# Performance work log

Measured on AMD Instinct MI355X. Metric: run time of the kernel, lower is better.

The kernel has to match this reference:

```python
import jax, jax.numpy as jnp
import numpy as np

T_IN, T_OUT = 16, 25          # in_length, out_length
B, K = 4096, 32               # heroes, neighbors per hero
N = B * K                     # total neighbor tracks
ENC, DEC, DYN, EMB = 64, 128, 32, 32


def _lrelu(x):
    return jnp.where(x >= 0, x, 0.1 * x)


def _lstm(x, Wih, Whh, bih, bhh, hidden):
    """PyTorch-convention LSTM (gate order i,f,g,o). x: [T, B, D]. Returns (all_h [T,B,H], last_h [B,H])."""
    z = jnp.zeros((x.shape[1], hidden), x.dtype)

    def step(carry, xt):
        h, c = carry
        g = xt @ Wih.T + bih + h @ Whh.T + bhh
        i, f, gg, o = jnp.split(g, 4, axis=-1)
        c = jax.nn.sigmoid(f) * c + jax.nn.sigmoid(i) * jnp.tanh(gg)
        h = jax.nn.sigmoid(o) * jnp.tanh(c)
        return (h, c), h

    (h, c), hs = jax.lax.scan(step, (z, z), x)
    return hs, h


def setup_inputs() -> dict:
    key = jax.random.key(0)
    ks = jax.random.split(key, 20)
    p = lambda k, s: jax.random.normal(k, s, jnp.float32) * 0.1
    return {
        "hist": jax.random.normal(ks[0], (T_IN, B, 2), jnp.float32),
        "nbrs": jax.random.normal(ks[1], (T_IN, N, 2), jnp.float32),
        "Wip": p(ks[2], (EMB, 2)), "bip": p(ks[3], (EMB,)),
        "Wih_e": p(ks[4], (4 * ENC, EMB)), "Whh_e": p(ks[5], (4 * ENC, ENC)),
        "bih_e": p(ks[6], (4 * ENC,)), "bhh_e": p(ks[7], (4 * ENC,)),
        "Wdyn": p(ks[8], (DYN, ENC)), "bdyn": p(ks[9], (DYN,)),
        "Wnbr": p(ks[10], (ENC, 2 * T_IN)), "bnbr": p(ks[11], (ENC,)),
        "Wih_d": p(ks[12], (4 * DEC, 2 * DYN)), "Whh_d": p(ks[13], (4 * DEC, DEC)),
        "bih_d": p(ks[14], (4 * DEC,)), "bhh_d": p(ks[15], (4 * DEC,)),
        "Wop": p(ks[16], (2, DEC)), "bop": p(ks[17], (2,)),
        # index_division flattened: neighbor j belongs to hero segment_ids[j] (sorted, K per hero)
        "segment_ids": jnp.repeat(jnp.arange(B, dtype=jnp.int32), K),
    }


def reference(hist, nbrs, Wip, bip, Wih_e, Whh_e, bih_e, bhh_e, Wdyn, bdyn,
              Wnbr, bnbr, Wih_d, Whh_d, bih_d, bhh_d, Wop, bop, segment_ids):
    # --- encode ego history ---
    emb = _lrelu(hist @ Wip.T + bip)                       # [T,B,EMB]
    _, h_enc = _lstm(emb, Wih_e, Whh_e, bih_e, bhh_e, ENC)  # [B,ENC]
    hist_e = _lrelu(h_enc @ Wdyn.T + bdyn)                 # [B,DYN]

    # --- relative neighbor tracks + ragged segment-max pooling ---
    relative = hist[:, segment_ids, :] - nbrs              # [T,N,2]  (hero_repeated gather)
    rela = jnp.transpose(relative, (1, 0, 2)).reshape(N, 2 * T_IN)  # permute(1,0,2).view(-1,2*in_length)
    rela_enc = _lrelu(rela @ Wnbr.T + bnbr)                # [N,ENC]
    scene = jax.ops.segment_max(rela_enc, segment_ids, num_segments=B)  # fused per-group max
    scene = _lrelu(scene @ Wdyn.T + bdyn)                  # [B,DYN]

    # --- decode ---
    enc = jnp.concatenate([hist_e, scene], axis=1)         # [B,2*DYN]
    dec_in = jnp.broadcast_to(enc, (T_OUT, B, 2 * DYN))    # unsqueeze(0).repeat(out_length,1,1)
    h_dec, _ = _lstm(dec_in, Wih_d, Whh_d, bih_d, bhh_d, DEC)  # [T_OUT,B,DEC]
    fut = h_dec @ Wop.T + bop                              # [T_OUT,B,2]
    # outputActivation: with 2 output dims (muX,muY only) it is the identity
    return fut
```

## Files before the change

kernel.cpp:

```cpp
#include <hip/hip_runtime.h>
#include <hip/hip_bf16.h>

#define T_IN   16
#define T_OUT  25
#define BHERO  4096
#define K_NBR  32
#define N_NBR  (BHERO * K_NBR)
#define ENC    64
#define DEC    128
#define DYN    32
#define EMB    32

#define EROW   104
#define DROW   136
#define RROW   40
#define SLABE  (16 * EROW * 2)
#define SLABD  (16 * DROW * 2)

#define OFF_RELA   56576
#define OFF_PMAX   97536
#define OFF_ENC    113152
#define OFF_WOP    117504
#define OFF_WIP    118528
#define OFF_BIP    118784
#define OFF_BOP    118912
#define LDS_TOTAL  118928

#define L2E 1.44269504f

typedef __attribute__((ext_vector_type(8))) short bf16x8;
typedef __attribute__((ext_vector_type(4))) float f32x4;

__device__ __forceinline__ float lrelu(float x) { return x >= 0.f ? x : 0.1f * x; }
__device__ __forceinline__ float rcpf(float x)  { return __builtin_amdgcn_rcpf(x); }
__device__ __forceinline__ float ex2(float x)   { return __builtin_amdgcn_exp2f(x); }
__device__ __forceinline__ unsigned pk2(float lo, float hi) {
    __hip_bfloat162 p = __float22bfloat162_rn(make_float2(lo, hi));
    unsigned u; __builtin_memcpy(&u, &p, 4); return u;
}
__device__ __forceinline__ bf16x8 mk_frag(float4 f0, float4 f1) {
    uint4 v = { pk2(f0.x, f0.y), pk2(f0.z, f0.w), pk2(f1.x, f1.y), pk2(f1.z, f1.w) };
    bf16x8 r; __builtin_memcpy(&r, &v, 16); return r;
}
__device__ __forceinline__ bf16x8 mk_frag_s(float4 f0, float4 f1, float s) {
    uint4 v = { pk2(f0.x*s, f0.y*s), pk2(f0.z*s, f0.w*s), pk2(f1.x*s, f1.y*s), pk2(f1.z*s, f1.w*s) };
    bf16x8 r; __builtin_memcpy(&r, &v, 16); return r;
}
__device__ __forceinline__ float bf2f(short s) {
    return __uint_as_float(((unsigned)(unsigned short)s) << 16);
}
__device__ __forceinline__ float2 cell_update(float gi, float gf, float gg, float go, float c) {
    float ea = ex2(-gi);
    float ef = ex2(-gf);
    float eb = ex2(-gg);
    float eo = ex2(-go);
    float ff = rcpf(1.f + ef);
    float ig = (1.f - eb) * rcpf((1.f + ea) * (1.f + eb));
    float cc = fmaf(ff, c, ig);
    float ec = ex2(-2.f * L2E * cc);
    float h  = (1.f - ec) * rcpf((1.f + eo) * (1.f + ec));
    return make_float2(h, cc);
}

__global__ __launch_bounds__(512, 2) void highway_fused(
    const float* __restrict__ hist,  const float* __restrict__ nbrs,
    const float* __restrict__ Wip,   const float* __restrict__ bip,
    const float* __restrict__ WihE,  const float* __restrict__ WhhE,
    const float* __restrict__ bihE,  const float* __restrict__ bhhE,
    const float* __restrict__ Wdyn,  const float* __restrict__ bdyn,
    const float* __restrict__ Wnbr,  const float* __restrict__ bnbr,
    const float* __restrict__ WihD,  const float* __restrict__ WhhD,
    const float* __restrict__ bihD,  const float* __restrict__ bhhD,
    const float* __restrict__ Wop,   const float* __restrict__ bop,
    const int*   __restrict__ seg,
    float* __restrict__ fut)
{
    __shared__ __align__(16) char lds_raw[LDS_TOTAL];
    auto slab   = (short (*)[16][EROW])  lds_raw;
    auto rela   = (short (*)[RROW])     (lds_raw + OFF_RELA);
    auto pmax   = (float (*)[ENC])      (lds_raw + OFF_PMAX);
    auto hist_s = (short (*)[16][DROW])  lds_raw;
    auto enc_s  = (float (*)[68])       (lds_raw + OFF_ENC);
    auto wop_s  = (float (*)[DEC])      (lds_raw + OFF_WOP);
    auto wip_s  = (float (*)[2])        (lds_raw + OFF_WIP);
    auto bip_s  = (float*)              (lds_raw + OFF_BIP);
    auto bop_s  = (float*)              (lds_raw + OFF_BOP);

    const int b0  = blockIdx.x * 16;
    const int n0  = blockIdx.x * 512;
    const int tid = threadIdx.x;
    const int w = tid >> 6, l = tid & 63, r = l & 15, lg = l >> 4;

    if (tid < EMB) {
        wip_s[tid][0] = Wip[2 * tid];
        wip_s[tid][1] = Wip[2 * tid + 1];
        bip_s[tid]    = bip[tid];
    }
    if (tid < 2 * DEC) wop_s[tid >> 7][tid & 127] = Wop[tid];
    if (tid < 2)       bop_s[tid] = bop[tid];
    for (int i = tid; i < 16 * ENC; i += 512) slab[0][i >> 6][32 + (i & 63)] = 0;

    bf16x8 BfE[4][3];
    float  biasE[4];
    bf16x8 BfN[2];
    float  biasn[2] = {0.f, 0.f};
    if (tid < 256) {
        #pragma unroll
        for (int j = 0; j < 4; ++j) {
            const float sj  = (j == 2) ? (2.f * L2E) : L2E;
            const int   col = j * ENC + w * 16 + r;
            biasE[j] = (bihE[col] + bhhE[col]) * sj;
            #pragma unroll
            for (int c = 0; c < 3; ++c) {
                const float* src = (c == 0) ? (WihE + (size_t)col * EMB + 8 * lg)
                                            : (WhhE + (size_t)col * ENC + (c - 1) * 32 + 8 * lg);
                BfE[j][c] = mk_frag_s(*(const float4*)src, *(const float4*)(src + 4), sj);
            }
        }
    } else {
        const int i = w - 4;
        const int ct0 = (i & 1) * 2;
        #pragma unroll
        for (int cc2 = 0; cc2 < 2; ++cc2) {
            const int col = (ct0 + cc2) * 16 + r;
            biasn[cc2] = bnbr[col];
            const float* src = Wnbr + (size_t)col * (2 * T_IN) + 8 * lg;
            BfN[cc2] = mk_frag(*(const float4*)src, *(const float4*)(src + 4));
        }
    }
    __syncthreads();

    if (tid < 256) {
        const int t = tid >> 4, m = tid & 15;
        float2 hv = *(const float2*)&hist[((size_t)t * BHERO + b0 + m) * 2];
        #pragma unroll
        for (int jb = 0; jb < 4; ++jb) {
            float e[8];
            #pragma unroll
            for (int q = 0; q < 8; ++q) {
                int j = jb * 8 + q;
                e[q] = lrelu(hv.x * wip_s[j][0] + hv.y * wip_s[j][1] + bip_s[j]);
            }
            uint4 v = { pk2(e[0],e[1]), pk2(e[2],e[3]), pk2(e[4],e[5]), pk2(e[6],e[7]) };
            __builtin_memcpy(&slab[t][m][jb * 8], &v, 16);
        }
    } else {
        const int x = tid - 256;
        const int n  = x & 31;
        const int ts = x >> 5;
        const int hb = seg[n0 + n];
        float2 h0 = *(const float2*)&hist[((size_t)ts * BHERO + hb) * 2];
        float2 v0 = *(const float2*)&nbrs[((size_t)ts * N_NBR + n0 + n) * 2];
        float2 h1 = *(const float2*)&hist[((size_t)(ts + 8) * BHERO + hb) * 2];
        float2 v1 = *(const float2*)&nbrs[((size_t)(ts + 8) * N_NBR + n0 + n) * 2];
        unsigned* dst = (unsigned*)&rela[n][0];
        dst[ts]     = pk2(h0.x - v0.x, h0.y - v0.y);
        dst[ts + 8] = pk2(h1.x - v1.x, h1.y - v1.y);
    }
    f32x4 cstE = {0.f, 0.f, 0.f, 0.f};
    __syncthreads();

    {
        const char* rbase = lds_raw + (size_t)r * (EROW * 2);
        char*       wbase = lds_raw + SLABE + (size_t)(4 * lg) * (EROW * 2) + (size_t)(32 + w * 16 + r) * 2;
        const int   x = tid - 256;
        #pragma unroll 1
        for (int t = 0; t < T_IN; ++t) {
            if (tid < 256) {
                const short* rp = (const short*)rbase;
                bf16x8 a0 = *(const bf16x8*)(rp + (0 + lg) * 8);
                bf16x8 a1 = *(const bf16x8*)(rp + (4 + lg) * 8);
                bf16x8 a2 = *(const bf16x8*)(rp + (8 + lg) * 8);
                f32x4 acc[4];
                #pragma unroll
                for (int j = 0; j < 4; ++j) {
                    f32x4 aA = (f32x4){biasE[j], biasE[j], biasE[j], biasE[j]};
                    f32x4 aB = (f32x4){0.f, 0.f, 0.f, 0.f};
                    aA = __builtin_amdgcn_mfma_f32_16x16x32_bf16(a0, BfE[j][0], aA, 0, 0, 0);
                    aB = __builtin_amdgcn_mfma_f32_16x16x32_bf16(a1, BfE[j][1], aB, 0, 0, 0);
                    aA = __builtin_amdgcn_mfma_f32_16x16x32_bf16(a2, BfE[j][2], aA, 0, 0, 0);
                    acc[j] = aA + aB;
                }
                float hq[4];
                #pragma unroll
                for (int q = 0; q < 4; ++q) {
                    float2 hc = cell_update(acc[0][q], acc[1][q], acc[2][q], acc[3][q], cstE[q]);
                    hq[q]   = hc.x;
                    cstE[q] = hc.y;
                }
                unsigned u01 = pk2(hq[0], hq[1]), u23 = pk2(hq[2], hq[3]);
                short* wp = (short*)wbase;
                wp[0 * EROW] = (short)u01; wp[1 * EROW] = (short)(u01 >> 16);
                wp[2 * EROW] = (short)u23; wp[3 * EROW] = (short)(u23 >> 16);
            } else {
                if (t < T_IN - 1) {
                    const int n  = 32 * (t + 1) + (x & 31);
                    const int ts = x >> 5;
                    const int hb = seg[n0 + n];
                    float2 h0 = *(const float2*)&hist[((size_t)ts * BHERO + hb) * 2];
                    float2 v0 = *(const float2*)&nbrs[((size_t)ts * N_NBR + n0 + n) * 2];
                    float2 h1 = *(const float2*)&hist[((size_t)(ts + 8) * BHERO + hb) * 2];
                    float2 v1 = *(const float2*)&nbrs[((size_t)(ts + 8) * N_NBR + n0 + n) * 2];
                    unsigned* dst = (unsigned*)&rela[n][0];
                    dst[ts]     = pk2(h0.x - v0.x, h0.y - v0.y);
                    dst[ts + 8] = pk2(h1.x - v1.x, h1.y - v1.y);
                }
                const int i  = w - 4;
                const int rt = 2 * t + (i >> 1);
                const int ct0 = (i & 1) * 2;
                bf16x8 a = *(const bf16x8*)&rela[rt * 16 + r][8 * lg];
                #pragma unroll
                for (int cc2 = 0; cc2 < 2; ++cc2) {
                    f32x4 acc = {biasn[cc2], biasn[cc2], biasn[cc2], biasn[cc2]};
                    acc = __builtin_amdgcn_mfma_f32_16x16x32_bf16(a, BfN[cc2], acc, 0, 0, 0);
                    float m4 = fmaxf(fmaxf(acc[0], acc[1]), fmaxf(acc[2], acc[3]));
                    m4 = fmaxf(m4, __shfl_xor(m4, 16));
                    m4 = fmaxf(m4, __shfl_xor(m4, 32));
                    if (l < 16) pmax[rt][(ct0 + cc2) * 16 + r] = m4;
                }
            }
            __syncthreads();
            rbase += SLABE; wbase += SLABE;
        }
    }

    #pragma unroll
    for (int it = 0; it < 2; ++it) {
        const int s = tid + 512 * it;
        const int m = s >> 6, col = s & 63;
        const float* wd = Wdyn + (size_t)(col & 31) * ENC;
        float a = bdyn[col & 31];
        if (col < 32) {
            const short* hp = &slab[T_IN][m][32];
            #pragma unroll
            for (int kb = 0; kb < 8; ++kb) {
                bf16x8 hv = *(const bf16x8*)(hp + kb * 8);
                #pragma unroll
                for (int e = 0; e < 8; ++e)
                    a = fmaf(bf2f(hv[e]), wd[kb * 8 + e], a);
            }
        } else {
            #pragma unroll
            for (int kb = 0; kb < 16; ++kb) {
                float4 p0 = *(const float4*)&pmax[2 * m][kb * 4];
                float4 p1 = *(const float4*)&pmax[2 * m + 1][kb * 4];
                a = fmaf(lrelu(fmaxf(p0.x, p1.x)), wd[kb * 4 + 0], a);
                a = fmaf(lrelu(fmaxf(p0.y, p1.y)), wd[kb * 4 + 1], a);
                a = fmaf(lrelu(fmaxf(p0.z, p1.z)), wd[kb * 4 + 2], a);
                a = fmaf(lrelu(fmaxf(p0.w, p1.w)), wd[kb * 4 + 3], a);
            }
        }
        enc_s[m][col] = lrelu(a);
    }
    for (int i = tid; i < 16 * DROW; i += 512) ((short*)hist_s)[i] = 0;
    __syncthreads();

    const int u0 = w * 16;
    bf16x8 BfD[4][4];
    float  biasD[4];
    float  sjD[4];
    #pragma unroll
    for (int j = 0; j < 4; ++j) {
        const float sj  = (j == 2) ? (2.f * L2E) : L2E;
        const int   col = j * DEC + u0 + r;
        sjD[j]   = sj;
        biasD[j] = (bihD[col] + bhhD[col]) * sj;
        #pragma unroll
        for (int c = 0; c < 4; ++c) {
            const float* src = WhhD + (size_t)col * DEC + c * 32 + 8 * lg;
            BfD[j][c] = mk_frag_s(*(const float4*)src, *(const float4*)(src + 4), sj);
        }
    }
    f32x4 xwf[4];
    {
        bf16x8 aE[2];
        #pragma unroll
        for (int c = 0; c < 2; ++c) {
            float4 f0 = *(const float4*)&enc_s[r][c * 32 + 8 * lg];
            float4 f1 = *(const float4*)&enc_s[r][c * 32 + 8 * lg + 4];
            aE[c] = mk_frag(f0, f1);
        }
        #pragma unroll
        for (int j = 0; j < 4; ++j) {
            const int col = j * DEC + u0 + r;
            f32x4 a = {biasD[j], biasD[j], biasD[j], biasD[j]};
            #pragma unroll
            for (int c = 0; c < 2; ++c) {
                const float* src = WihD + (size_t)col * (2 * DYN) + c * 32 + 8 * lg;
                a = __builtin_amdgcn_mfma_f32_16x16x32_bf16(
                        aE[c], mk_frag_s(*(const float4*)src, *(const float4*)(src + 4), sjD[j]),
                        a, 0, 0, 0);
            }
            xwf[j] = a;
        }
    }

    f32x4 cst = {0.f, 0.f, 0.f, 0.f};
    {
        const char* rbase = lds_raw + (size_t)r * (DROW * 2);
        char*       wbase = lds_raw + SLABD + (size_t)(4 * lg) * (DROW * 2) + (size_t)(u0 + r) * 2;
        #pragma unroll 1
        for (int t = 0; t < T_OUT; ++t) {
            const short* rp = (const short*)rbase;
            bf16x8 a_[4];
            #pragma unroll
            for (int c = 0; c < 4; ++c)
                a_[c] = *(const bf16x8*)(rp + (4 * c + lg) * 8);
            f32x4 acc[4];
            #pragma unroll
            for (int j = 0; j < 4; ++j) {
                f32x4 aA = xwf[j];
                f32x4 aB = (f32x4){0.f, 0.f, 0.f, 0.f};
                aA = __builtin_amdgcn_mfma_f32_16x16x32_bf16(a_[0], BfD[j][0], aA, 0, 0, 0);
                aB = __builtin_amdgcn_mfma_f32_16x16x32_bf16(a_[1], BfD[j][1], aB, 0, 0, 0);
                aA = __builtin_amdgcn_mfma_f32_16x16x32_bf16(a_[2], BfD[j][2], aA, 0, 0, 0);
                aB = __builtin_amdgcn_mfma_f32_16x16x32_bf16(a_[3], BfD[j][3], aB, 0, 0, 0);
                acc[j] = aA + aB;
            }
            float hq[4];
            #pragma unroll
            for (int q = 0; q < 4; ++q) {
                float2 hc = cell_update(acc[0][q], acc[1][q], acc[2][q], acc[3][q], cst[q]);
                hq[q]  = hc.x;
                cst[q] = hc.y;
            }
            unsigned u01 = pk2(hq[0], hq[1]), u23 = pk2(hq[2], hq[3]);
            short* wp = (short*)wbase;
            wp[0 * DROW] = (short)u01; wp[1 * DROW] = (short)(u01 >> 16);
            wp[2 * DROW] = (short)u23; wp[3 * DROW] = (short)(u23 >> 16);
            __syncthreads();
            rbase += SLABD; wbase += SLABD;
        }
    }

    {
        bf16x8 Bop[4];
        #pragma unroll
        for (int c = 0; c < 4; ++c) {
            float wv[8];
            #pragma unroll
            for (int e = 0; e < 8; ++e)
                wv[e] = (r < 2) ? wop_s[r][c * 32 + 8 * lg + e] : 0.f;
            uint4 v = { pk2(wv[0],wv[1]), pk2(wv[2],wv[3]), pk2(wv[4],wv[5]), pk2(wv[6],wv[7]) };
            __builtin_memcpy(&Bop[c], &v, 16);
        }
        const float bopr = (r < 2) ? bop_s[r] : 0.f;
        #pragma unroll 1
        for (int t = w; t < T_OUT; t += 8) {
            const short* rp = &hist_s[t + 1][r][0];
            bf16x8 a_[4];
            #pragma unroll
            for (int c = 0; c < 4; ++c)
                a_[c] = *(const bf16x8*)(rp + (4 * c + lg) * 8);
            f32x4 acc = {0.f, 0.f, 0.f, 0.f};
            #pragma unroll
            for (int c = 0; c < 4; ++c)
                acc = __builtin_amdgcn_mfma_f32_16x16x32_bf16(a_[c], Bop[c], acc, 0, 0, 0);
            if (r < 2) {
                #pragma unroll
                for (int q = 0; q < 4; ++q)
                    fut[((size_t)t * BHERO + b0 + 4 * lg + q) * 2 + r] = acc[q] + bopr;
            }
        }
    }
}

extern "C" void kernel_launch(void* const* d_in, const int* in_sizes, int n_in,
                              void* d_out, int out_size, void* d_ws, size_t ws_size,
                              hipStream_t stream) {
    (void)d_ws; (void)ws_size; (void)in_sizes; (void)n_in; (void)out_size;
    const float* hist  = (const float*)d_in[0];
    const float* nbrs  = (const float*)d_in[1];
    const float* Wip   = (const float*)d_in[2];
    const float* bip   = (const float*)d_in[3];
    const float* Wih_e = (const float*)d_in[4];
    const float* Whh_e = (const float*)d_in[5];
    const float* bih_e = (const float*)d_in[6];
    const float* bhh_e = (const float*)d_in[7];
    const float* Wdyn  = (const float*)d_in[8];
    const float* bdyn  = (const float*)d_in[9];
    const float* Wnbr  = (const float*)d_in[10];
    const float* bnbr  = (const float*)d_in[11];
    const float* Wih_d = (const float*)d_in[12];
    const float* Whh_d = (const float*)d_in[13];
    const float* bih_d = (const float*)d_in[14];
    const float* bhh_d = (const float*)d_in[15];
    const float* Wop   = (const float*)d_in[16];
    const float* bop   = (const float*)d_in[17];
    const int*   seg   = (const int*)d_in[18];
    float* fut = (float*)d_out;

    hipLaunchKernelGGL(highway_fused, dim3(BHERO / 16), dim3(512), 0, stream,
                       hist, nbrs, Wip, bip, Wih_e, Whh_e, bih_e, bhh_e, Wdyn, bdyn,
                       Wnbr, bnbr, Wih_d, Whh_d, bih_d, bhh_d, Wop, bop, seg, fut);
}
```

Baseline: 61.76 us.

## Shrink per-block heroes to 8 with ring buffers to raise occupancy

Each block now handles 8 heroes instead of 16. Hidden-state slabs are replaced with double-buffered ring buffers, which cuts LDS from about 119KB to 46KB so launch bounds can request 4 blocks per CU and the grid doubles. The 16-row MFMA tiles are filled by duplicating rows, so half of the MFMA work is redundant. Neighbor loads are software-pipelined two steps ahead, and the output projection is folded into the decoder loop, one wave per step.

```diff
diff --git a/kernel.cpp b/kernel.cpp
--- a/kernel.cpp
+++ b/kernel.cpp
@@ -10,21 +10,23 @@
 #define DEC    128
 #define DYN    32
 #define EMB    32
-
-#define EROW   104
+#define HEROES 8
+
+#define EMROW  40
+#define HROW   72
+#define RROW   40
 #define DROW   136
-#define RROW   40
-#define SLABE  (16 * EROW * 2)
-#define SLABD  (16 * DROW * 2)
-
-#define OFF_RELA   56576
-#define OFF_PMAX   97536
-#define OFF_ENC    113152
-#define OFF_WOP    117504
-#define OFF_WIP    118528
-#define OFF_BIP    118784
-#define OFF_BOP    118912
-#define LDS_TOTAL  118928
+
+#define OFF_HRING  20480
+#define OFF_RELA   25088
+#define OFF_PMAX   27648
+#define OFF_RINGD  31744
+#define OFF_ENC    40448
+#define OFF_WOP    44800
+#define OFF_WIP    45824
+#define OFF_BIP    46080
+#define OFF_BOP    46208
+#define LDS_TOTAL  46216
 
 #define L2E 1.44269504f
 
@@ -62,7 +64,7 @@
     return make_float2(h, cc);
 }
 
-__global__ __launch_bounds__(512, 2) void highway_fused(
+__global__ __launch_bounds__(512, 4) void highway_fused(
     const float* __restrict__ hist,  const float* __restrict__ nbrs,
     const float* __restrict__ Wip,   const float* __restrict__ bip,
     const float* __restrict__ WihE,  const float* __restrict__ WhhE,
@@ -76,18 +78,19 @@
     float* __restrict__ fut)
 {
     __shared__ __align__(16) char lds_raw[LDS_TOTAL];
-    auto slab   = (short (*)[16][EROW])  lds_raw;
-    auto rela   = (short (*)[RROW])     (lds_raw + OFF_RELA);
-    auto pmax   = (float (*)[ENC])      (lds_raw + OFF_PMAX);
-    auto hist_s = (short (*)[16][DROW])  lds_raw;
-    auto enc_s  = (float (*)[68])       (lds_raw + OFF_ENC);
-    auto wop_s  = (float (*)[DEC])      (lds_raw + OFF_WOP);
-    auto wip_s  = (float (*)[2])        (lds_raw + OFF_WIP);
-    auto bip_s  = (float*)              (lds_raw + OFF_BIP);
-    auto bop_s  = (float*)              (lds_raw + OFF_BOP);
-
-    const int b0  = blockIdx.x * 16;
-    const int n0  = blockIdx.x * 512;
+    auto embs   = (short (*)[16][EMROW])  lds_raw;
+    auto hringE = (short (*)[16][HROW])  (lds_raw + OFF_HRING);
+    auto rela2  = (short (*)[16][RROW])  (lds_raw + OFF_RELA);
+    auto pmax   = (float (*)[ENC])       (lds_raw + OFF_PMAX);
+    auto ringD  = (short (*)[16][DROW])  (lds_raw + OFF_RINGD);
+    auto enc_s  = (float (*)[68])        (lds_raw + OFF_ENC);
+    auto wop_s  = (float (*)[DEC])       (lds_raw + OFF_WOP);
+    auto wip_s  = (float (*)[2])         (lds_raw + OFF_WIP);
+    auto bip_s  = (float*)               (lds_raw + OFF_BIP);
+    auto bop_s  = (float*)               (lds_raw + OFF_BOP);
+
+    const int b0  = blockIdx.x * HEROES;
+    const int n0  = blockIdx.x * (HEROES * K_NBR);
     const int tid = threadIdx.x;
     const int w = tid >> 6, l = tid & 63, r = l & 15, lg = l >> 4;
 
@@ -98,12 +101,12 @@
     }
     if (tid < 2 * DEC) wop_s[tid >> 7][tid & 127] = Wop[tid];
     if (tid < 2)       bop_s[tid] = bop[tid];
-    for (int i = tid; i < 16 * ENC; i += 512) slab[0][i >> 6][32 + (i & 63)] = 0;
+    for (int i = tid; i < 16 * HROW; i += 512) ((short*)hringE[0])[i] = 0;
 
     bf16x8 BfE[4][3];
     float  biasE[4];
-    bf16x8 BfN[2];
-    float  biasn[2] = {0.f, 0.f};
+    bf16x8 BfN;
+    float  biasn = 0.f;
     if (tid < 256) {
         #pragma unroll
         for (int j = 0; j < 4; ++j) {
@@ -118,59 +121,64 @@
             }
         }
     } else {
-        const int i = w - 4;
-        const int ct0 = (i & 1) * 2;
-        #pragma unroll
-        for (int cc2 = 0; cc2 < 2; ++cc2) {
-            const int col = (ct0 + cc2) * 16 + r;
-            biasn[cc2] = bnbr[col];
-            const float* src = Wnbr + (size_t)col * (2 * T_IN) + 8 * lg;
-            BfN[cc2] = mk_frag(*(const float4*)src, *(const float4*)(src + 4));
-        }
+        const int col = (w - 4) * 16 + r;
+        biasn = bnbr[col];
+        const float* src = Wnbr + (size_t)col * (2 * T_IN) + 8 * lg;
+        BfN = mk_frag(*(const float4*)src, *(const float4*)(src + 4));
     }
     __syncthreads();
 
+    float2 c_h0 = {}, c_v0 = {};
+    int    sg_c = 0;
     if (tid < 256) {
-        const int t = tid >> 4, m = tid & 15;
+        const int task = tid >> 1;
+        const int t = task >> 3, m = task & 7;
+        const int j0 = (tid & 1) * 16;
         float2 hv = *(const float2*)&hist[((size_t)t * BHERO + b0 + m) * 2];
         #pragma unroll
-        for (int jb = 0; jb < 4; ++jb) {
+        for (int jb = 0; jb < 2; ++jb) {
             float e[8];
             #pragma unroll
             for (int q = 0; q < 8; ++q) {
-                int j = jb * 8 + q;
+                int j = j0 + jb * 8 + q;
                 e[q] = lrelu(hv.x * wip_s[j][0] + hv.y * wip_s[j][1] + bip_s[j]);
             }
             uint4 v = { pk2(e[0],e[1]), pk2(e[2],e[3]), pk2(e[4],e[5]), pk2(e[6],e[7]) };
-            __builtin_memcpy(&slab[t][m][jb * 8], &v, 16);
+            __builtin_memcpy(&embs[t][m][j0 + jb * 8], &v, 16);
+            __builtin_memcpy(&embs[t][m + 8][j0 + jb * 8], &v, 16);
         }
     } else {
-        const int x = tid - 256;
-        const int n  = x & 31;
-        const int ts = x >> 5;
-        const int hb = seg[n0 + n];
-        float2 h0 = *(const float2*)&hist[((size_t)ts * BHERO + hb) * 2];
-        float2 v0 = *(const float2*)&nbrs[((size_t)ts * N_NBR + n0 + n) * 2];
-        float2 h1 = *(const float2*)&hist[((size_t)(ts + 8) * BHERO + hb) * 2];
-        float2 v1 = *(const float2*)&nbrs[((size_t)(ts + 8) * N_NBR + n0 + n) * 2];
-        unsigned* dst = (unsigned*)&rela[n][0];
-        dst[ts]     = pk2(h0.x - v0.x, h0.y - v0.y);
-        dst[ts + 8] = pk2(h1.x - v1.x, h1.y - v1.y);
+        const int x    = tid - 256;
+        const int nloc = x & 15;
+        const int ts   = x >> 4;
+        {
+            const int hb = seg[n0 + nloc];
+            float2 h0 = *(const float2*)&hist[((size_t)ts * BHERO + hb) * 2];
+            float2 v0 = *(const float2*)&nbrs[((size_t)ts * N_NBR + n0 + nloc) * 2];
+            ((unsigned*)&rela2[0][nloc][0])[ts] = pk2(h0.x - v0.x, h0.y - v0.y);
+        }
+        {
+            const int n  = 16 + nloc;
+            const int hb = seg[n0 + n];
+            c_h0 = *(const float2*)&hist[((size_t)ts * BHERO + hb) * 2];
+            c_v0 = *(const float2*)&nbrs[((size_t)ts * N_NBR + n0 + n) * 2];
+        }
+        sg_c = seg[n0 + 32 + nloc];
     }
     f32x4 cstE = {0.f, 0.f, 0.f, 0.f};
     __syncthreads();
 
     {
-        const char* rbase = lds_raw + (size_t)r * (EROW * 2);
-        char*       wbase = lds_raw + SLABE + (size_t)(4 * lg) * (EROW * 2) + (size_t)(32 + w * 16 + r) * 2;
-        const int   x = tid - 256;
+        const int x    = tid - 256;
+        const int nloc = x & 15;
+        const int ts   = x >> 4;
         #pragma unroll 1
         for (int t = 0; t < T_IN; ++t) {
+            const int cur = t & 1, nxt = cur ^ 1;
             if (tid < 256) {
-                const short* rp = (const short*)rbase;
-                bf16x8 a0 = *(const bf16x8*)(rp + (0 + lg) * 8);
-                bf16x8 a1 = *(const bf16x8*)(rp + (4 + lg) * 8);
-                bf16x8 a2 = *(const bf16x8*)(rp + (8 + lg) * 8);
+                bf16x8 a0 = *(const bf16x8*)&embs[t][r][8 * lg];
+                bf16x8 a1 = *(const bf16x8*)&hringE[cur][r][8 * lg];
+                bf16x8 a2 = *(const bf16x8*)&hringE[cur][r][32 + 8 * lg];
                 f32x4 acc[4];
                 #pragma unroll
                 for (int j = 0; j < 4; ++j) {
@@ -189,49 +197,39 @@
                     cstE[q] = hc.y;
                 }
                 unsigned u01 = pk2(hq[0], hq[1]), u23 = pk2(hq[2], hq[3]);
-                short* wp = (short*)wbase;
-                wp[0 * EROW] = (short)u01; wp[1 * EROW] = (short)(u01 >> 16);
-                wp[2 * EROW] = (short)u23; wp[3 * EROW] = (short)(u23 >> 16);
+                short* wp = &hringE[nxt][4 * lg][w * 16 + r];
+                wp[0 * HROW] = (short)u01; wp[1 * HROW] = (short)(u01 >> 16);
+                wp[2 * HROW] = (short)u23; wp[3 * HROW] = (short)(u23 >> 16);
             } else {
-                if (t < T_IN - 1) {
-                    const int n  = 32 * (t + 1) + (x & 31);
-                    const int ts = x >> 5;
-                    const int hb = seg[n0 + n];
-                    float2 h0 = *(const float2*)&hist[((size_t)ts * BHERO + hb) * 2];
-                    float2 v0 = *(const float2*)&nbrs[((size_t)ts * N_NBR + n0 + n) * 2];
-                    float2 h1 = *(const float2*)&hist[((size_t)(ts + 8) * BHERO + hb) * 2];
-                    float2 v1 = *(const float2*)&nbrs[((size_t)(ts + 8) * N_NBR + n0 + n) * 2];
-                    unsigned* dst = (unsigned*)&rela[n][0];
-                    dst[ts]     = pk2(h0.x - v0.x, h0.y - v0.y);
-                    dst[ts + 8] = pk2(h1.x - v1.x, h1.y - v1.y);
+                float2 n_h0 = {}, n_v0 = {};
+                int    sg_n = 0;
+                if (t < T_IN - 2) {
+                    const int n = 16 * (t + 2) + nloc;
+                    n_h0 = *(const float2*)&hist[((size_t)ts * BHERO + sg_c) * 2];
+                    n_v0 = *(const float2*)&nbrs[((size_t)ts * N_NBR + n0 + n) * 2];
                 }
-                const int i  = w - 4;
-                const int rt = 2 * t + (i >> 1);
-                const int ct0 = (i & 1) * 2;
-                bf16x8 a = *(const bf16x8*)&rela[rt * 16 + r][8 * lg];
-                #pragma unroll
-                for (int cc2 = 0; cc2 < 2; ++cc2) {
-                    f32x4 acc = {biasn[cc2], biasn[cc2], biasn[cc2], biasn[cc2]};
-                    acc = __builtin_amdgcn_mfma_f32_16x16x32_bf16(a, BfN[cc2], acc, 0, 0, 0);
-                    float m4 = fmaxf(fmaxf(acc[0], acc[1]), fmaxf(acc[2], acc[3]));
-                    m4 = fmaxf(m4, __shfl_xor(m4, 16));
-                    m4 = fmaxf(m4, __shfl_xor(m4, 32));
-                    if (l < 16) pmax[rt][(ct0 + cc2) * 16 + r] = m4;
-                }
+                if (t < T_IN - 3) sg_n = seg[n0 + 16 * (t + 3) + nloc];
+                if (t < T_IN - 1)
+                    ((unsigned*)&rela2[nxt][nloc][0])[ts] = pk2(c_h0.x - c_v0.x, c_h0.y - c_v0.y);
+                bf16x8 a = *(const bf16x8*)&rela2[cur][r][8 * lg];
+                f32x4 acc = {biasn, biasn, biasn, biasn};
+                acc = __builtin_amdgcn_mfma_f32_16x16x32_bf16(a, BfN, acc, 0, 0, 0);
+                float m4 = fmaxf(fmaxf(acc[0], acc[1]), fmaxf(acc[2], acc[3]));
+                m4 = fmaxf(m4, __shfl_xor(m4, 16));
+                m4 = fmaxf(m4, __shfl_xor(m4, 32));
+                if (l < 16) pmax[t][(w - 4) * 16 + r] = m4;
+                c_h0 = n_h0; c_v0 = n_v0; sg_c = sg_n;
             }
             __syncthreads();
-            rbase += SLABE; wbase += SLABE;
-        }
-    }
-
-    #pragma unroll
-    for (int it = 0; it < 2; ++it) {
-        const int s = tid + 512 * it;
-        const int m = s >> 6, col = s & 63;
+        }
+    }
+
+    {
+        const int m = tid >> 6, col = tid & 63;
         const float* wd = Wdyn + (size_t)(col & 31) * ENC;
         float a = bdyn[col & 31];
         if (col < 32) {
-            const short* hp = &slab[T_IN][m][32];
+            const short* hp = &hringE[0][m][0];
             #pragma unroll
             for (int kb = 0; kb < 8; ++kb) {
                 bf16x8 hv = *(const bf16x8*)(hp + kb * 8);
@@ -250,20 +248,20 @@
                 a = fmaf(lrelu(fmaxf(p0.w, p1.w)), wd[kb * 4 + 3], a);
             }
         }
-        enc_s[m][col] = lrelu(a);
-    }
-    for (int i = tid; i < 16 * DROW; i += 512) ((short*)hist_s)[i] = 0;
+        float av = lrelu(a);
+        enc_s[m][col]     = av;
+        enc_s[m + 8][col] = av;
+        for (int i = tid; i < 16 * DROW; i += 512) ((short*)ringD[0])[i] = 0;
+    }
     __syncthreads();
 
     const int u0 = w * 16;
     bf16x8 BfD[4][4];
     float  biasD[4];
-    float  sjD[4];
     #pragma unroll
     for (int j = 0; j < 4; ++j) {
         const float sj  = (j == 2) ? (2.f * L2E) : L2E;
         const int   col = j * DEC + u0 + r;
-        sjD[j]   = sj;
         biasD[j] = (bihD[col] + bhhD[col]) * sj;
         #pragma unroll
         for (int c = 0; c < 4; ++c) {
@@ -282,13 +280,14 @@
         }
         #pragma unroll
         for (int j = 0; j < 4; ++j) {
-            const int col = j * DEC + u0 + r;
+            const float sj  = (j == 2) ? (2.f * L2E) : L2E;
+            const int   col = j * DEC + u0 + r;
             f32x4 a = {biasD[j], biasD[j], biasD[j], biasD[j]};
             #pragma unroll
             for (int c = 0; c < 2; ++c) {
                 const float* src = WihD + (size_t)col * (2 * DYN) + c * 32 + 8 * lg;
                 a = __builtin_amdgcn_mfma_f32_16x16x32_bf16(
-                        aE[c], mk_frag_s(*(const float4*)src, *(const float4*)(src + 4), sjD[j]),
+                        aE[c], mk_frag_s(*(const float4*)src, *(const float4*)(src + 4), sj),
                         a, 0, 0, 0);
             }
             xwf[j] = a;
@@ -296,71 +295,78 @@
     }
 
     f32x4 cst = {0.f, 0.f, 0.f, 0.f};
-    {
-        const char* rbase = lds_raw + (size_t)r * (DROW * 2);
-        char*       wbase = lds_raw + SLABD + (size_t)(4 * lg) * (DROW * 2) + (size_t)(u0 + r) * 2;
-        #pragma unroll 1
-        for (int t = 0; t < T_OUT; ++t) {
-            const short* rp = (const short*)rbase;
-            bf16x8 a_[4];
-            #pragma unroll
-            for (int c = 0; c < 4; ++c)
-                a_[c] = *(const bf16x8*)(rp + (4 * c + lg) * 8);
-            f32x4 acc[4];
-            #pragma unroll
-            for (int j = 0; j < 4; ++j) {
-                f32x4 aA = xwf[j];
-                f32x4 aB = (f32x4){0.f, 0.f, 0.f, 0.f};
-                aA = __builtin_amdgcn_mfma_f32_16x16x32_bf16(a_[0], BfD[j][0], aA, 0, 0, 0);
-                aB = __builtin_amdgcn_mfma_f32_16x16x32_bf16(a_[1], BfD[j][1], aB, 0, 0, 0);
-                aA = __builtin_amdgcn_mfma_f32_16x16x32_bf16(a_[2], BfD[j][2], aA, 0, 0, 0);
-                aB = __builtin_amdgcn_mfma_f32_16x16x32_bf16(a_[3], BfD[j][3], aB, 0, 0, 0);
-                acc[j] = aA + aB;
-            }
-            float hq[4];
-            #pragma unroll
-            for (int q = 0; q < 4; ++q) {
-                float2 hc = cell_update(acc[0][q], acc[1][q], acc[2][q], acc[3][q], cst[q]);
-                hq[q]  = hc.x;
-                cst[q] = hc.y;
-            }
-            unsigned u01 = pk2(hq[0], hq[1]), u23 = pk2(hq[2], hq[3]);
-            short* wp = (short*)wbase;
-            wp[0 * DROW] = (short)u01; wp[1 * DROW] = (short)(u01 >> 16);
-            wp[2 * DROW] = (short)u23; wp[3 * DROW] = (short)(u23 >> 16);
-            __syncthreads();
-            rbase += SLABD; wbase += SLABD;
-        }
-    }
-
-    {
-        bf16x8 Bop[4];
-        #pragma unroll
-        for (int c = 0; c < 4; ++c) {
-            float wv[8];
-            #pragma unroll
-            for (int e = 0; e < 8; ++e)
-                wv[e] = (r < 2) ? wop_s[r][c * 32 + 8 * lg + e] : 0.f;
-            uint4 v = { pk2(wv[0],wv[1]), pk2(wv[2],wv[3]), pk2(wv[4],wv[5]), pk2(wv[6],wv[7]) };
-            __builtin_memcpy(&Bop[c], &v, 16);
-        }
-        const float bopr = (r < 2) ? bop_s[r] : 0.f;
-        #pragma unroll 1
-        for (int t = w; t < T_OUT; t += 8) {
-            const short* rp = &hist_s[t + 1][r][0];
-            bf16x8 a_[4];
-            #pragma unroll
-            for (int c = 0; c < 4; ++c)
-                a_[c] = *(const bf16x8*)(rp + (4 * c + lg) * 8);
-            f32x4 acc = {0.f, 0.f, 0.f, 0.f};
-            #pragma unroll
-            for (int c = 0; c < 4; ++c)
-                acc = __builtin_amdgcn_mfma_f32_16x16x32_bf16(a_[c], Bop[c], acc, 0, 0, 0);
-            if (r < 2) {
+    #pragma unroll 1
+    for (int t = 0; t < T_OUT; ++t) {
+        const int cur = t & 1, nxt = cur ^ 1;
+        const short* rp = &ringD[cur][r][0];
+        bf16x8 a_[4];
+        #pragma unroll
+        for (int c = 0; c < 4; ++c)
+            a_[c] = *(const bf16x8*)(rp + (4 * c + lg) * 8);
+        f32x4 acc[4];
+        #pragma unroll
+        for (int j = 0; j < 4; ++j) {
+            f32x4 aA = xwf[j];
+            f32x4 aB = (f32x4){0.f, 0.f, 0.f, 0.f};
+            aA = __builtin_amdgcn_mfma_f32_16x16x32_bf16(a_[0], BfD[j][0], aA, 0, 0, 0);
+            aB = __builtin_amdgcn_mfma_f32_16x16x32_bf16(a_[1], BfD[j][1], aB, 0, 0, 0);
+            aA = __builtin_amdgcn_mfma_f32_16x16x32_bf16(a_[2], BfD[j][2], aA, 0, 0, 0);
+            aB = __builtin_amdgcn_mfma_f32_16x16x32_bf16(a_[3], BfD[j][3], aB, 0, 0, 0);
+            acc[j] = aA + aB;
+        }
+        if (t >= 1 && w == ((t - 1) & 7)) {
+            f32x4 accO = {0.f, 0.f, 0.f, 0.f};
+            #pragma unroll
+            for (int c = 0; c < 4; ++c) {
+                bf16x8 bo = (bf16x8){0, 0, 0, 0, 0, 0, 0, 0};
+                if (r < 2) {
+                    float4 f0 = *(const float4*)&wop_s[r][c * 32 + 8 * lg];
+                    float4 f1 = *(const float4*)&wop_s[r][c * 32 + 8 * lg + 4];
+                    bo = mk_frag(f0, f1);
+                }
+                accO = __builtin_amdgcn_mfma_f32_16x16x32_bf16(a_[c], bo, accO, 0, 0, 0);
+            }
+            if (r < 2 && lg < 2) {
                 #pragma unroll
                 for (int q = 0; q < 4; ++q)
-                    fut[((size_t)t * BHERO + b0 + 4 * lg + q) * 2 + r] = acc[q] + bopr;
-            }
+                    fut[((size_t)(t - 1) * BHERO + b0 + 4 * lg + q) * 2 + r] = accO[q] + bop_s[r];
+            }
+        }
+        float hq[4];
+        #pragma unroll
+        for (int q = 0; q < 4; ++q) {
+            float2 hc = cell_update(acc[0][q], acc[1][q], acc[2][q], acc[3][q], cst[q]);
+            hq[q]  = hc.x;
+            cst[q] = hc.y;
+        }
+        unsigned u01 = pk2(hq[0], hq[1]), u23 = pk2(hq[2], hq[3]);
+        short* wp = &ringD[nxt][4 * lg][u0 + r];
+        wp[0 * DROW] = (short)u01; wp[1 * DROW] = (short)(u01 >> 16);
+        wp[2 * DROW] = (short)u23; wp[3 * DROW] = (short)(u23 >> 16);
+        __syncthreads();
+    }
+
+    if (w == ((T_OUT - 1) & 7)) {
+        const short* rp = &ringD[T_OUT & 1][r][0];
+        bf16x8 a_[4];
+        #pragma unroll
+        for (int c = 0; c < 4; ++c)
+            a_[c] = *(const bf16x8*)(rp + (4 * c + lg) * 8);
+        f32x4 accO = {0.f, 0.f, 0.f, 0.f};
+        #pragma unroll
+        for (int c = 0; c < 4; ++c) {
+            bf16x8 bo = (bf16x8){0, 0, 0, 0, 0, 0, 0, 0};
+            if (r < 2) {
+                float4 f0 = *(const float4*)&wop_s[r][c * 32 + 8 * lg];
+                float4 f1 = *(const float4*)&wop_s[r][c * 32 + 8 * lg + 4];
+                bo = mk_frag(f0, f1);
+            }
+            accO = __builtin_amdgcn_mfma_f32_16x16x32_bf16(a_[c], bo, accO, 0, 0, 0);
+        }
+        if (r < 2 && lg < 2) {
+            #pragma unroll
+            for (int q = 0; q < 4; ++q)
+                fut[((size_t)(T_OUT - 1) * BHERO + b0 + 4 * lg + q) * 2 + r] = accO[q] + bop_s[r];
         }
     }
 }
@@ -390,7 +396,7 @@
     const int*   seg   = (const int*)d_in[18];
     float* fut = (float*)d_out;
 
-    hipLaunchKernelGGL(highway_fused, dim3(BHERO / 16), dim3(512), 0, stream,
+    hipLaunchKernelGGL(highway_fused, dim3(BHERO / HEROES), dim3(512), 0, stream,
                        hist, nbrs, Wip, bip, Wih_e, Whh_e, bih_e, bhh_e, Wdyn, bdyn,
                        Wnbr, bnbr, Wih_d, Whh_d, bih_d, bhh_d, Wop, bop, seg, fut);
 }
```

New measurement: 150.3 us. 143% more time.
